# Kernel optimization log

Hardware: AMD Instinct MI355X
Metric: run time of the kernel (lower is better)

The kernel has to match this reference:

```python
import jax, jax.numpy as jnp
import numpy as np

T = 1.0  # temperature

def _free_energy(v, W, b, c):
    # v: [B, V]; W: [V, H]; b: [V]; c: [H]
    vW = v @ W                                  # [B, H]
    W_colsum = W.sum(axis=0)                    # [H]
    negF_normal = (v * b).sum(-1) - jax.nn.softplus(vW + c).sum(-1)
    negF_flip = ((1.0 - v) * b).sum(-1) - jax.nn.softplus(W_colsum - vW + c).sum(-1)
    negF = jnp.stack([negF_normal, negF_flip], axis=-1)  # [B, 2]
    return -T * jax.nn.logsumexp(negF / T, axis=-1)      # [B]

def _gibbs_chain(v0, W, b, c, key, k):
    B = v0.shape[0]
    key, k0 = jax.random.split(key)
    u0 = jax.random.bernoulli(k0, 0.5, (B, 1)).astype(v0.dtype)
    b_sum = b.sum()

    def step(carry, _):
        v, u, key = carry
        key, k1, k2, k3 = jax.random.split(key, 4)
        v_branch = u * v + (1.0 - u) * (1.0 - v)
        h = jax.random.bernoulli(k1, jax.nn.sigmoid(v_branch @ W + c)).astype(v.dtype)  # [B,H]
        a = h @ W.T                                                                     # [B,V]
        vb = (v * b).sum(-1)
        va = (v * a).sum(-1)
        dE = -b_sum - a.sum(-1) + 2.0 * vb + 2.0 * va
        u_new = jax.random.bernoulli(k2, jax.nn.sigmoid(dE)).astype(v.dtype)[:, None]
        v_new = jax.random.bernoulli(k3, jax.nn.sigmoid(a + b)).astype(v.dtype)
        v = u_new * v_new + (1.0 - u_new) * (1.0 - v_new)
        return (v, u_new, key), None

    (v_model, _, _), _ = jax.lax.scan(step, (v0, u0, key), None, length=k)
    return v_model

def setup_inputs() -> dict:
    key = jax.random.key(0)
    kv, kw = jax.random.split(key)
    B, V, H = 8192, 1024, 1024
    v_data = jnp.round(jax.random.uniform(kv, (B, V), dtype=jnp.float32))  # binary 0/1
    W = 0.01 * jax.random.normal(kw, (V, H), dtype=jnp.float32)
    b = jnp.zeros((V,), dtype=jnp.float32)
    c = jnp.zeros((H,), dtype=jnp.float32)
    return {"v_data": v_data, "W": W, "b": b, "c": c, "seed": 0}

def reference(v_data, W, b, c, seed):
    K = 10  # Gibbs steps
    key = jax.random.key(seed)
    v_model = _gibbs_chain(v_data, W, b, c, key, K)
    v_model = jax.lax.stop_gradient(v_model)  # .detach() in torch
    loss = _free_energy(v_data, W, b, c).mean() - _free_energy(v_model, W, b, c).mean()
    return loss
```

## Files before the change

### kernel.cpp

```cpp
#include <hip/hip_runtime.h>
#include <hip/hip_bf16.h>
#include <stdint.h>
#include <math.h>


static constexpr int Bn = 8192;
static constexpr int Vn = 1024;
static constexpr int Hn = 1024;
static constexpr int KSTEPS = 10;

typedef _Float16 f16;
typedef f16   f16x4 __attribute__((ext_vector_type(4)));
typedef f16   f16x8 __attribute__((ext_vector_type(8)));
typedef float f32x4 __attribute__((ext_vector_type(4)));

#define GLOBAL_LOAD_LDS16(g, l)                                              \
  __builtin_amdgcn_global_load_lds(                                          \
      (const __attribute__((address_space(1))) uint32_t*)(g),                \
      (__attribute__((address_space(3))) uint32_t*)(l), 16, 0, 0)

__device__ __forceinline__ uint32_t rotl32(uint32_t x, int d) {
  return (x << d) | (x >> (32 - d));
}

__device__ __forceinline__ void tf2x32(uint32_t k0, uint32_t k1,
                                       uint32_t x0, uint32_t x1,
                                       uint32_t& o0, uint32_t& o1) {
  uint32_t k2 = k0 ^ k1 ^ 0x1BD11BDAu;
#define TFR(r) { x0 += x1; x1 = rotl32(x1, (r)); x1 ^= x0; }
  x0 += k0; x1 += k1;
  TFR(13) TFR(15) TFR(26) TFR(6)
  x0 += k1; x1 += k2 + 1u;
  TFR(17) TFR(29) TFR(16) TFR(24)
  x0 += k2; x1 += k0 + 2u;
  TFR(13) TFR(15) TFR(26) TFR(6)
  x0 += k0; x1 += k1 + 3u;
  TFR(17) TFR(29) TFR(16) TFR(24)
  x0 += k1; x1 += k2 + 4u;
  TFR(13) TFR(15) TFR(26) TFR(6)
  x0 += k2; x1 += k0 + 5u;
#undef TFR
  o0 = x0; o1 = x1;
}

__device__ __forceinline__ float rng_u01(uint2 key, uint32_t idx) {
  uint32_t o0, o1;
  tf2x32(key.x, key.y, 0u, idx, o0, o1);
  uint32_t bits = o0 ^ o1;
  return __uint_as_float((bits >> 9) | 0x3F800000u) - 1.0f;
}

__device__ __attribute__((noinline)) float4 rng4_u01(uint2 key, uint32_t i0,
                                                     uint32_t i1, uint32_t i2,
                                                     uint32_t i3) {
  float4 r;
  r.x = rng_u01(key, i0);
  r.y = rng_u01(key, i1);
  r.z = rng_u01(key, i2);
  r.w = rng_u01(key, i3);
  return r;
}

__device__ __forceinline__ float bern_fast(float z, float r01) {
  float e = __expf(-z);
  return (__builtin_fmaf(r01, e, r01) < 1.0f) ? 1.f : 0.f;
}
__device__ __forceinline__ float softplus_fast(float x) {
  return fmaxf(x, 0.f) + __logf(1.f + __expf(-fabsf(x)));
}

template <int CTRL>
__device__ __forceinline__ float dpp_add16(float v) {
  int x = __builtin_amdgcn_update_dpp(0, __float_as_int(v), CTRL, 0xF, 0xF, true);
  return v + __int_as_float(x);
}
__device__ __forceinline__ float red16(float v) {
  v = dpp_add16<0xB1>(v);
  v = dpp_add16<0x4E>(v);
  v = dpp_add16<0x141>(v);
  v = dpp_add16<0x140>(v);
  return v;
}

__global__ void prep_keys(const int* __restrict__ seedp, uint2* __restrict__ keys) {
  if (threadIdx.x != 0 || blockIdx.x != 0) return;
  uint32_t seed = (uint32_t)(*seedp);
  uint2 key = make_uint2(0u, seed);
  uint2 nk, kk;
  tf2x32(key.x, key.y, 0u, 0u, nk.x, nk.y);
  tf2x32(key.x, key.y, 0u, 1u, kk.x, kk.y);
  keys[0] = kk;
  key = nk;
  for (int s = 0; s < KSTEPS; ++s) {
    uint2 t0, t1, t2, t3;
    tf2x32(key.x, key.y, 0u, 0u, t0.x, t0.y);
    tf2x32(key.x, key.y, 0u, 1u, t1.x, t1.y);
    tf2x32(key.x, key.y, 0u, 2u, t2.x, t2.y);
    tf2x32(key.x, key.y, 0u, 3u, t3.x, t3.y);
    key = t0;
    keys[1 + 3*s] = t1;
    keys[2 + 3*s] = t2;
    keys[3 + 3*s] = t3;
  }
}

__global__ __launch_bounds__(256) void colsum_part(
    const float* __restrict__ W, float* __restrict__ part) {
  const int bx = blockIdx.x, t = threadIdx.x;
  float s0 = 0.f, s1 = 0.f, s2 = 0.f, s3 = 0.f;
#pragma unroll
  for (int r = 0; r < 16; ++r) {
    const float* row = W + (size_t)(bx * 16 + r) * Hn;
    s0 += row[t]; s1 += row[t + 256]; s2 += row[t + 512]; s3 += row[t + 768];
  }
  float* p = part + (size_t)bx * Hn;
  p[t] = s0; p[t + 256] = s1; p[t + 512] = s2; p[t + 768] = s3;
}

__global__ __launch_bounds__(256) void colsum_red(
    const float* __restrict__ part, float* __restrict__ cs) {
  const int col = blockIdx.x * 256 + threadIdx.x;
  float s = 0.f;
#pragma unroll
  for (int k = 0; k < 64; ++k) s += part[(size_t)k * Hn + col];
  cs[col] = s;
}

__global__ void bsum_k(const float* __restrict__ bvec, float* __restrict__ bs) {
  __shared__ float sb[4];
  float s = 0.f;
  for (int i = threadIdx.x; i < Vn; i += 256) s += bvec[i];
  for (int off = 32; off > 0; off >>= 1) s += __shfl_down(s, off, 64);
  int wv = threadIdx.x >> 6, ln = threadIdx.x & 63;
  if (ln == 0) sb[wv] = s;
  __syncthreads();
  if (threadIdx.x == 0) bs[0] = sb[0] + sb[1] + sb[2] + sb[3];
}

__global__ __launch_bounds__(256) void cast_W(
    const float* __restrict__ W, f16* __restrict__ Wf, f16* __restrict__ WTf) {
  __shared__ f16 tile[64][65];
  const int j0 = blockIdx.x * 64, i0 = blockIdx.y * 64;
  const int tx = threadIdx.x & 63, tg = threadIdx.x >> 6;
#pragma unroll 4
  for (int rr = 0; rr < 16; ++rr) {
    const int row = tg * 16 + rr;
    float w = W[(size_t)(i0 + row) * Hn + j0 + tx];
    f16 hw = (f16)w;
    Wf[(size_t)(i0 + row) * Hn + j0 + tx] = hw;
    tile[row][tx] = hw;
  }
  __syncthreads();
#pragma unroll 4
  for (int rr = 0; rr < 16; ++rr) {
    const int row = tg * 16 + rr;
    WTf[(size_t)(j0 + row) * Vn + i0 + tx] = tile[tx][row];
  }
}

__global__ void u0_init(const uint2* __restrict__ keys, float* __restrict__ u0) {
  int b = blockIdx.x * 256 + threadIdx.x;
  float r01 = rng_u01(keys[0], (uint32_t)b);
  u0[b] = (r01 < 0.5f) ? 1.f : 0.f;
}

__global__ __launch_bounds__(256) void cast_vx(
    const float* __restrict__ vd, const float* __restrict__ u0,
    const float* __restrict__ bvec, f16* __restrict__ x,
    float* __restrict__ pXB0) {
  const int row = blockIdx.x;
  const int t = threadIdx.x;
  const float uo = u0[row];
  const float4 d  = ((const float4*)(vd + (size_t)row * Vn))[t];
  const float4 bv = ((const float4*)bvec)[t];
  float xv[4] = { d.x, d.y, d.z, d.w };
  if (uo <= 0.5f) { xv[0]=1.f-xv[0]; xv[1]=1.f-xv[1]; xv[2]=1.f-xv[2]; xv[3]=1.f-xv[3]; }
  f16x4 o = { (f16)xv[0], (f16)xv[1], (f16)xv[2], (f16)xv[3] };
  *(f16x4*)(x + (size_t)row * Vn + t * 4) = o;
  float xb = xv[0]*bv.x + xv[1]*bv.y + xv[2]*bv.z + xv[3]*bv.w;
#pragma unroll
  for (int m = 1; m < 8; m <<= 1) xb += __shfl_xor(xb, m, 64);
  if ((t & 7) == 0) pXB0[(size_t)row * 32 + (t >> 3)] = xb;
}

template <int EPI>
__global__ __launch_bounds__(256, 2) void gemm_s(
    const f16* __restrict__ A, const f16* __restrict__ Bm,
    f16* __restrict__ outH, f16* __restrict__ xnew,
    const float* __restrict__ bvec, const float* __restrict__ cvec,
    const float* __restrict__ colsum,
    float* __restrict__ pA, float* __restrict__ pXA, float* __restrict__ pXBn,
    float* __restrict__ pSA, float* __restrict__ pSB,
    const uint2* __restrict__ keys, int keyIdx)
{
  constexpr int N = 1024, K = 1024, BK = 64;
  __shared__ alignas(16) f16 As[2][128 * BK];
  __shared__ alignas(16) f16 Bs[2][128 * BK];

  const int t = threadIdx.x, wave = t >> 6, lane = t & 63;
  const int l15 = lane & 15, quad = lane >> 4;
  const int m0 = blockIdx.x * 128, n0 = blockIdx.y * 128;
  const int wm = (wave >> 1) * 64, wn = (wave & 1) * 64;

  const int rbase = lane >> 3;
  const int gch   = (lane & 7) ^ rbase;
  const f16* gA = A  + (size_t)(m0 + wave * 32 + rbase) * K + gch * 8;
  const f16* gB = Bm + (size_t)(n0 + wave * 32 + rbase) * K + gch * 8;
  const int woff = wave * 32 * BK;

  const int swz = l15 & 7;
  const int oA  = (wm + l15) * BK;
  const int oB  = (wn + l15) * BK;

  uint2 key = make_uint2(0u, 0u);
  if constexpr (EPI != 4) key = keys[keyIdx];

  f32x4 acc[4][4] = {};
  float r01v[64];

#pragma unroll
  for (int i = 0; i < 4; ++i) {
    GLOBAL_LOAD_LDS16(gA + i * 8 * K, As[0] + woff + i * 8 * BK);
    GLOBAL_LOAD_LDS16(gB + i * 8 * K, Bs[0] + woff + i * 8 * BK);
  }
  __syncthreads();

#pragma unroll
  for (int ki = 0; ki < 16; ++ki) {
    const int cur = ki & 1;
    if (ki < 15) {
      const int k0n = (ki + 1) * 64;
      f16* wA = (cur ? As[0] : As[1]) + woff;
      f16* wB = (cur ? Bs[0] : Bs[1]) + woff;
#pragma unroll
      for (int i = 0; i < 4; ++i) {
        GLOBAL_LOAD_LDS16(gA + k0n + i * 8 * K, wA + i * 8 * BK);
        GLOBAL_LOAD_LDS16(gB + k0n + i * 8 * K, wB + i * 8 * BK);
      }
    }
    if constexpr (EPI != 4) {
      uint32_t idx[4];
#pragma unroll
      for (int j = 0; j < 4; ++j) {
        const int e  = ki * 4 + j;
        const int mt = e >> 4, r = (e >> 2) & 3, nt = e & 3;
        const int gm = m0 + wm + mt * 16 + quad * 4 + r;
        const int gn = n0 + wn + nt * 16 + l15;
        idx[j] = (uint32_t)(gm * N + gn);
      }
      float4 rv = rng4_u01(key, idx[0], idx[1], idx[2], idx[3]);
      r01v[ki * 4 + 0] = rv.x;
      r01v[ki * 4 + 1] = rv.y;
      r01v[ki * 4 + 2] = rv.z;
      r01v[ki * 4 + 3] = rv.w;
    }
    const f16* rA = cur ? As[1] : As[0];
    const f16* rB = cur ? Bs[1] : Bs[0];
#pragma unroll
    for (int kc = 0; kc < 2; ++kc) {
      const int fc = ((kc * 4 + quad) ^ swz) * 8;
      f16x8 af[4], bf[4];
#pragma unroll
      for (int i = 0; i < 4; ++i) {
        af[i] = *(const f16x8*)(&rA[oA + i * 16 * BK + fc]);
        bf[i] = *(const f16x8*)(&rB[oB + i * 16 * BK + fc]);
      }
#pragma unroll
      for (int mt = 0; mt < 4; ++mt)
#pragma unroll
        for (int nt = 0; nt < 4; ++nt)
          acc[mt][nt] = __builtin_amdgcn_mfma_f32_16x16x32_f16(af[mt], bf[nt], acc[mt][nt], 0, 0, 0);
    }
    if (ki < 15) __syncthreads();
  }

  const int slotBase = blockIdx.y * 4 + (wave & 1) * 2;

  if constexpr (EPI == 1 || EPI == 2) {
    float csv[4], cvv[4];
#pragma unroll
    for (int nt = 0; nt < 4; ++nt) {
      const int gn = n0 + wn + nt * 16 + l15;
      csv[nt] = colsum[gn];
      cvv[nt] = cvec[gn];
    }
#pragma unroll
    for (int mt = 0; mt < 4; ++mt)
#pragma unroll
      for (int r = 0; r < 4; ++r) {
        const int gm = m0 + wm + mt * 16 + quad * 4 + r;
#pragma unroll
        for (int p = 0; p < 2; ++p) {
          float pa = 0.f, pxa = 0.f, sa = 0.f, sb = 0.f;
#pragma unroll
          for (int q = 0; q < 2; ++q) {
            const int nt = p * 2 + q;
            const int gn = n0 + wn + nt * 16 + l15;
            const float val = acc[mt][nt][r];
            const float r01 = r01v[mt * 16 + r * 4 + nt];
            float hq  = bern_fast(val + cvv[nt], r01);
            outH[(size_t)gm * N + gn] = (f16)hq;
            pa  += hq * csv[nt];
            pxa += hq * val;
            if constexpr (EPI == 2) {
              sa += softplus_fast(val + cvv[nt]);
              sb += softplus_fast(csv[nt] - val + cvv[nt]);
            }
          }
          pa  = red16(pa);
          pxa = red16(pxa);
          if constexpr (EPI == 2) {
            sa = red16(sa);
            sb = red16(sb);
          }
          if (l15 == 0) {
            pA [(size_t)gm * 32 + slotBase + p] = pa;
            pXA[(size_t)gm * 32 + slotBase + p] = pxa;
            if constexpr (EPI == 2) {
              pSA[(size_t)gm * 32 + slotBase + p] = sa;
              pSB[(size_t)gm * 32 + slotBase + p] = sb;
            }
          }
        }
      }
  } else if constexpr (EPI == 3) {
    float bb[4];
#pragma unroll
    for (int nt = 0; nt < 4; ++nt) bb[nt] = bvec[n0 + wn + nt * 16 + l15];
#pragma unroll
    for (int mt = 0; mt < 4; ++mt)
#pragma unroll
      for (int r = 0; r < 4; ++r) {
        const int gm = m0 + wm + mt * 16 + quad * 4 + r;
#pragma unroll
        for (int p = 0; p < 2; ++p) {
          float pxb = 0.f;
#pragma unroll
          for (int q = 0; q < 2; ++q) {
            const int nt = p * 2 + q;
            const int gn = n0 + wn + nt * 16 + l15;
            const float aval = acc[mt][nt][r];
            const float r01 = r01v[mt * 16 + r * 4 + nt];
            float xq  = bern_fast(aval + bb[nt], r01);
            xnew[(size_t)gm * N + gn] = (f16)xq;
            pxb += xq * bb[nt];
          }
          pxb = red16(pxb);
          if (l15 == 0) pXBn[(size_t)gm * 32 + slotBase + p] = pxb;
        }
      }
  } else {
    float csv[4], cvv[4];
#pragma unroll
    for (int nt = 0; nt < 4; ++nt) {
      const int gn = n0 + wn + nt * 16 + l15;
      csv[nt] = colsum[gn];
      cvv[nt] = cvec[gn];
    }
#pragma unroll
    for (int mt = 0; mt < 4; ++mt)
#pragma unroll
      for (int r = 0; r < 4; ++r) {
        const int gm = m0 + wm + mt * 16 + quad * 4 + r;
#pragma unroll
        for (int p = 0; p < 2; ++p) {
          float sa = 0.f, sb = 0.f;
#pragma unroll
          for (int q = 0; q < 2; ++q) {
            const int nt = p * 2 + q;
            const float val = acc[mt][nt][r];
            sa += softplus_fast(val + cvv[nt]);
            sb += softplus_fast(csv[nt] - val + cvv[nt]);
          }
          sa = red16(sa);
          sb = red16(sb);
          if (l15 == 0) {
            pSA[(size_t)gm * 32 + slotBase + p] = sa;
            pSB[(size_t)gm * 32 + slotBase + p] = sb;
          }
        }
      }
  }
}

__global__ __launch_bounds__(256) void u_chain(
    const float* __restrict__ pA, const float* __restrict__ pXA,
    const float* __restrict__ pXB, const float* __restrict__ bsum,
    const uint2* __restrict__ keys, const float* __restrict__ u0,
    float* __restrict__ uF)
{
  const int t = threadIdx.x, wave = t >> 6, lane = t & 63;
  const int r2 = lane >> 5, slot = lane & 31;
  const int row = blockIdx.x * 8 + wave * 2 + r2;
  const float bs = bsum[0];
  float uo = u0[row];
  for (int s = 0; s < KSTEPS; ++s) {
    const size_t o = (size_t)s * 32 * Bn + (size_t)row * 32 + slot;
    float sa  = pA [o];
    float sxa = pXA[o];
    float sxb = pXB[o];
#pragma unroll
    for (int m = 1; m < 32; m <<= 1) {
      sa  += __shfl_xor(sa,  m, 64);
      sxa += __shfl_xor(sxa, m, 64);
      sxb += __shfl_xor(sxb, m, 64);
    }
    const float va = (uo > 0.5f) ? sxa : sa - sxa;
    const float vb = (uo > 0.5f) ? sxb : bs - sxb;
    const float dE = -bs - sa + 2.f * vb + 2.f * va;
    uo = bern_fast(dE, rng_u01(keys[2 + 3 * s], (uint32_t)row));
  }
  if (slot == 0) uF[row] = uo;
}

__device__ __forceinline__ float fe_eval(float SA, float SB, float xb,
                                         float uo, float bs) {
  float S1 = (uo > 0.5f) ? SA : SB;
  float S2 = (uo > 0.5f) ? SB : SA;
  float vb = (uo > 0.5f) ? xb : bs - xb;
  float negn = vb - S1;
  float negf = (bs - vb) - S2;
  float mx = fmaxf(negn, negf);
  return -(mx + logf(expf(negn - mx) + expf(negf - mx)));
}

__global__ __launch_bounds__(256) void fe_finish(
    const float* __restrict__ SA0, const float* __restrict__ SB0,
    const float* __restrict__ xb0,
    const float* __restrict__ SAF, const float* __restrict__ SBF,
    const float* __restrict__ xbF,
    const float* __restrict__ u0, const float* __restrict__ uF,
    const float* __restrict__ bsum,
    float* __restrict__ Fd, float* __restrict__ Fm)
{
  const int t = threadIdx.x, wave = t >> 6, lane = t & 63;
  const int r2 = lane >> 5, slot = lane & 31;
  const int row = blockIdx.x * 8 + wave * 2 + r2;
  const size_t o = (size_t)row * 32 + slot;
  const float bs = bsum[0];
  float a0 = SA0[o], b0 = SB0[o], x0 = xb0[o];
  float aF = SAF[o], bF = SBF[o], xF = xbF[o];
#pragma unroll
  for (int m = 1; m < 32; m <<= 1) {
    a0 += __shfl_xor(a0, m, 64);  b0 += __shfl_xor(b0, m, 64);
    x0 += __shfl_xor(x0, m, 64);  aF += __shfl_xor(aF, m, 64);
    bF += __shfl_xor(bF, m, 64);  xF += __shfl_xor(xF, m, 64);
  }
  if (slot == 0) {
    Fd[row] = fe_eval(a0, b0, x0, u0[row], bs);
    Fm[row] = fe_eval(aF, bF, xF, uF[row], bs);
  }
}

__global__ __launch_bounds__(256) void finalize_k(
    const float* __restrict__ Fd, const float* __restrict__ Fm, float* __restrict__ out)
{
  __shared__ double sb[8];
  double sd = 0.0, sm = 0.0;
  for (int i = threadIdx.x; i < Bn; i += 256) { sd += (double)Fd[i]; sm += (double)Fm[i]; }
  for (int off = 32; off > 0; off >>= 1) { sd += __shfl_down(sd, off, 64); sm += __shfl_down(sm, off, 64); }
  const int wv = threadIdx.x >> 6, ln = threadIdx.x & 63;
  if (ln == 0) { sb[wv] = sd; sb[4 + wv] = sm; }
  __syncthreads();
  if (threadIdx.x == 0) {
    sd = sb[0] + sb[1] + sb[2] + sb[3];
    sm = sb[4] + sb[5] + sb[6] + sb[7];
    out[0] = (float)((sd - sm) / (double)Bn);
  }
}

extern "C" void kernel_launch(void* const* d_in, const int* in_sizes, int n_in,
                              void* d_out, int out_size, void* d_ws, size_t ws_size,
                              hipStream_t stream) {
  const float* v_data = (const float*)d_in[0];
  const float* W      = (const float*)d_in[1];
  const float* bvec   = (const float*)d_in[2];
  const float* cvec   = (const float*)d_in[3];
  const int*   seedp  = (const int*)d_in[4];
  float* out = (float*)d_out;

  char* ws = (char*)d_ws;
  size_t off = 0;
  auto alloc = [&](size_t bytes) -> void* {
    void* p = ws + off;
    off += (bytes + 255) & ~(size_t)255;
    return p;
  };
  f16*   xb0  = (f16*)alloc((size_t)Bn * Vn * 2);
  f16*   xb1  = (f16*)alloc((size_t)Bn * Vn * 2);
  f16*   h    = (f16*)alloc((size_t)Bn * Hn * 2);
  f16*   Wf   = (f16*)alloc((size_t)Vn * Hn * 2);
  f16*   WTf  = (f16*)alloc((size_t)Vn * Hn * 2);
  float* cpart  = (float*)alloc(64 * Hn * 4);
  float* colsum = (float*)alloc(Hn * 4);
  float* bsum   = (float*)alloc(256);
  uint2* keys   = (uint2*)alloc(64 * sizeof(uint2));
  float* u0     = (float*)alloc(Bn * 4);
  float* uF     = (float*)alloc(Bn * 4);
  float* pA     = (float*)alloc((size_t)KSTEPS * 32 * Bn * 4);
  float* pXA    = (float*)alloc((size_t)KSTEPS * 32 * Bn * 4);
  float* pXB    = (float*)alloc((size_t)(KSTEPS + 1) * 32 * Bn * 4);
  float* SA0    = (float*)alloc((size_t)32 * Bn * 4);
  float* SB0    = (float*)alloc((size_t)32 * Bn * 4);
  float* SAF    = (float*)alloc((size_t)32 * Bn * 4);
  float* SBF    = (float*)alloc((size_t)32 * Bn * 4);
  float* Fd     = (float*)alloc(Bn * 4);
  float* Fm     = (float*)alloc(Bn * 4);
  (void)ws_size; (void)in_sizes; (void)n_in; (void)out_size;

  prep_keys<<<1, 64, 0, stream>>>(seedp, keys);
  colsum_part<<<64, 256, 0, stream>>>(W, cpart);
  colsum_red<<<4, 256, 0, stream>>>(cpart, colsum);
  bsum_k<<<1, 256, 0, stream>>>(bvec, bsum);
  cast_W<<<dim3(Hn / 64, Vn / 64), 256, 0, stream>>>(W, Wf, WTf);
  u0_init<<<Bn / 256, 256, 0, stream>>>(keys, u0);
  cast_vx<<<Bn, 256, 0, stream>>>(v_data, u0, bvec, xb0, pXB);

  dim3 gg(Bn / 128, Hn / 128);
  f16* xs[2] = { xb0, xb1 };
  const size_t SL = (size_t)32 * Bn;

  for (int s = 0; s < KSTEPS; ++s) {
    if (s == 0) {
      gemm_s<2><<<gg, 256, 0, stream>>>(xs[0], WTf, h, nullptr, nullptr, cvec,
                                        colsum, pA, pXA, nullptr, SA0, SB0,
                                        keys, 1);
    } else {
      gemm_s<1><<<gg, 256, 0, stream>>>(xs[s & 1], WTf, h, nullptr, nullptr, cvec,
                                        colsum, pA + (size_t)s * SL,
                                        pXA + (size_t)s * SL, nullptr,
                                        nullptr, nullptr, keys, 1 + 3 * s);
    }
    gemm_s<3><<<gg, 256, 0, stream>>>(h, Wf, nullptr, xs[(s + 1) & 1], bvec,
                                      nullptr, nullptr, nullptr, nullptr,
                                      pXB + (size_t)(s + 1) * SL,
                                      nullptr, nullptr, keys, 3 + 3 * s);
  }

  gemm_s<4><<<gg, 256, 0, stream>>>(xs[KSTEPS & 1], WTf, nullptr, nullptr,
                                    nullptr, cvec, colsum, nullptr, nullptr,
                                    nullptr, SAF, SBF, keys, 0);

  u_chain<<<Bn / 8, 256, 0, stream>>>(pA, pXA, pXB, bsum, keys, u0, uF);
  fe_finish<<<Bn / 8, 256, 0, stream>>>(SA0, SB0, pXB,
                                        SAF, SBF, pXB + (size_t)KSTEPS * SL,
                                        u0, uF, bsum, Fd, Fm);
  finalize_k<<<1, 256, 0, stream>>>(Fd, Fm, out);
}
```

Baseline: 880.4 us.

## Prefetch two K-tiles ahead with register-staged fragments and partial vmcnt waits

```diff
diff --git a/kernel.cpp b/kernel.cpp
--- a/kernel.cpp
+++ b/kernel.cpp
@@ -220,18 +220,38 @@
 
 #pragma unroll
   for (int i = 0; i < 4; ++i) {
-    GLOBAL_LOAD_LDS16(gA + i * 8 * K, As[0] + woff + i * 8 * BK);
-    GLOBAL_LOAD_LDS16(gB + i * 8 * K, Bs[0] + woff + i * 8 * BK);
-  }
-  __syncthreads();
+    GLOBAL_LOAD_LDS16(gA + i * 8 * K,      As[0] + woff + i * 8 * BK);
+    GLOBAL_LOAD_LDS16(gB + i * 8 * K,      Bs[0] + woff + i * 8 * BK);
+  }
+#pragma unroll
+  for (int i = 0; i < 4; ++i) {
+    GLOBAL_LOAD_LDS16(gA + 64 + i * 8 * K, As[1] + woff + i * 8 * BK);
+    GLOBAL_LOAD_LDS16(gB + 64 + i * 8 * K, Bs[1] + woff + i * 8 * BK);
+  }
+  asm volatile("s_waitcnt vmcnt(8)" ::: "memory");
+  __builtin_amdgcn_s_barrier();
 
 #pragma unroll
   for (int ki = 0; ki < 16; ++ki) {
-    const int cur = ki & 1;
-    if (ki < 15) {
-      const int k0n = (ki + 1) * 64;
-      f16* wA = (cur ? As[0] : As[1]) + woff;
-      f16* wB = (cur ? Bs[0] : Bs[1]) + woff;
+    const f16* rA = As[ki & 1];
+    const f16* rB = Bs[ki & 1];
+    f16x8 af[2][4], bf[2][4];
+#pragma unroll
+    for (int kc = 0; kc < 2; ++kc) {
+      const int fc = ((kc * 4 + quad) ^ swz) * 8;
+#pragma unroll
+      for (int i = 0; i < 4; ++i) {
+        af[kc][i] = *(const f16x8*)(&rA[oA + i * 16 * BK + fc]);
+        bf[kc][i] = *(const f16x8*)(&rB[oB + i * 16 * BK + fc]);
+      }
+    }
+    asm volatile("s_waitcnt lgkmcnt(0)" ::: "memory");
+    __builtin_amdgcn_sched_barrier(0);
+    __builtin_amdgcn_s_barrier();
+    if (ki < 14) {
+      const int k0n = (ki + 2) * 64;
+      f16* wA = (f16*)As[ki & 1] + woff;
+      f16* wB = (f16*)Bs[ki & 1] + woff;
 #pragma unroll
       for (int i = 0; i < 4; ++i) {
         GLOBAL_LOAD_LDS16(gA + k0n + i * 8 * K, wA + i * 8 * BK);
@@ -254,24 +274,20 @@
       r01v[ki * 4 + 2] = rv.z;
       r01v[ki * 4 + 3] = rv.w;
     }
-    const f16* rA = cur ? As[1] : As[0];
-    const f16* rB = cur ? Bs[1] : Bs[0];
-#pragma unroll
-    for (int kc = 0; kc < 2; ++kc) {
-      const int fc = ((kc * 4 + quad) ^ swz) * 8;
-      f16x8 af[4], bf[4];
-#pragma unroll
-      for (int i = 0; i < 4; ++i) {
-        af[i] = *(const f16x8*)(&rA[oA + i * 16 * BK + fc]);
-        bf[i] = *(const f16x8*)(&rB[oB + i * 16 * BK + fc]);
-      }
+#pragma unroll
+    for (int kc = 0; kc < 2; ++kc)
 #pragma unroll
       for (int mt = 0; mt < 4; ++mt)
 #pragma unroll
         for (int nt = 0; nt < 4; ++nt)
-          acc[mt][nt] = __builtin_amdgcn_mfma_f32_16x16x32_f16(af[mt], bf[nt], acc[mt][nt], 0, 0, 0);
-    }
-    if (ki < 15) __syncthreads();
+          acc[mt][nt] = __builtin_amdgcn_mfma_f32_16x16x32_f16(af[kc][mt], bf[kc][nt], acc[mt][nt], 0, 0, 0);
+    if (ki < 14) {
+      asm volatile("s_waitcnt vmcnt(8)" ::: "memory");
+      __builtin_amdgcn_s_barrier();
+    } else if (ki == 14) {
+      asm volatile("s_waitcnt vmcnt(0)" ::: "memory");
+      __builtin_amdgcn_s_barrier();
+    }
   }
 
   const int slotBase = blockIdx.y * 4 + (wave & 1) * 2;
```

Result: slower. 933.0 us (+6.0%).
